# Kernel optimization log

Hardware: AMD Instinct MI355X
Metric: run time of the kernel (lower is better)

## Reference

```python
import jax, jax.numpy as jnp
import numpy as np

N = 100000       # nodes
DEG = 16         # in-degree per node
E = N * DEG      # edges
IN_DIM = 128
H_DIM = 128
NEG_SLOPE = 0.01  # F.leaky_relu default


def setup_inputs() -> dict:
    key = jax.random.key(0)
    ks = jax.random.split(key, 12)
    sc = 0.05
    attr = jax.random.normal(ks[0], (N, IN_DIM), jnp.float32)
    edge_d = jax.random.uniform(ks[1], (E, 1), dtype=jnp.float32)
    edge_src = jax.random.randint(ks[2], (E,), 0, N, dtype=jnp.int32)
    edge_dst = jnp.repeat(jnp.arange(N, dtype=jnp.int32), DEG)  # every node gets DEG msgs
    return {
        "attr": attr,
        "edge_d": edge_d,
        "W_V1": jax.random.normal(ks[3], (1, 1), jnp.float32) * sc,
        "W_W1": jax.random.normal(ks[4], (H_DIM, IN_DIM), jnp.float32) * sc,
        "W_U1": jax.random.normal(ks[5], (H_DIM, IN_DIM), jnp.float32) * sc,
        "W_a1": jax.random.normal(ks[6], (1, 2 * H_DIM + 1), jnp.float32) * sc,
        "W_V2": jax.random.normal(ks[7], (1, 1), jnp.float32) * sc,
        "W_W2": jax.random.normal(ks[8], (H_DIM, H_DIM), jnp.float32) * sc,
        "W_U2": jax.random.normal(ks[9], (H_DIM, H_DIM), jnp.float32) * sc,
        "W_a2": jax.random.normal(ks[10], (1, 2 * H_DIM + 1), jnp.float32) * sc,
        "edge_src": edge_src,
        "edge_dst": edge_dst,
    }


def gat_layer(h, edge_d, edge_src, edge_dst, W_V, W_W, W_U, W_a):
    n = h.shape[0]
    t = edge_d @ W_V.T                      # [E,1] edge feature transform (fcV)
    z = h @ W_W.T                           # [N,H] (fcW)
    z_i = h @ W_U.T                         # [N,H] (fcU)
    Hd = z.shape[1]
    a = W_a[0]                              # [2H+1]
    a_src, a_dst, a_t = a[:Hd], a[Hd:2 * Hd], a[2 * Hd:]
    # attn_fc(concat(z_src, z_dst, t)) decomposed into per-node scores + edge term
    s_src = z @ a_src                       # [N]
    s_dst = z @ a_dst                       # [N]
    e = s_src[edge_src] + s_dst[edge_dst] + (t @ a_t)  # [E]
    e = jax.nn.leaky_relu(e, NEG_SLOPE)
    # per-destination-node softmax over incoming edges (mailbox softmax)
    m = jax.ops.segment_max(e, edge_dst, num_segments=n)
    ex = jnp.exp(e - m[edge_dst])
    denom = jax.ops.segment_sum(ex, edge_dst, num_segments=n)
    alpha = ex / denom[edge_dst]            # [E]
    # weighted neighbor aggregation
    zn = jax.ops.segment_sum(alpha[:, None] * z[edge_src], edge_dst, num_segments=n)
    return jax.nn.relu(z_i + zn)


def reference(attr, edge_d, W_V1, W_W1, W_U1, W_a1, W_V2, W_W2, W_U2, W_a2,
              edge_src, edge_dst):
    h = gat_layer(attr, edge_d, edge_src, edge_dst, W_V1, W_W1, W_U1, W_a1)
    h = gat_layer(h, edge_d, edge_src, edge_dst, W_V2, W_W2, W_U2, W_a2)
    return h
```

## Files before the change

kernel.cpp:

```cpp
#include <hip/hip_runtime.h>

#define N_NODES 100000
#define DEG 16
#define DIM 128
#define NTILES 1563
#define T8 196
#define DGRID (T8 * 4 * 8)
#define LSTR 136

typedef short bf16x8 __attribute__((ext_vector_type(8)));
typedef float f32x4 __attribute__((ext_vector_type(4)));

__device__ __forceinline__ unsigned short f2bf(float f) {
    unsigned int u = __builtin_bit_cast(unsigned int, f);
    u = (u + 0x7fffu + ((u >> 16) & 1u)) >> 16;
    return (unsigned short)u;
}
__device__ __forceinline__ float bf2f(unsigned short h) {
    unsigned int u = ((unsigned int)h) << 16;
    return __builtin_bit_cast(float, u);
}
__device__ __forceinline__ bf16x8 pack_bf16x8(float4 lo, float4 hi) {
    bf16x8 f;
    f[0] = (short)f2bf(lo.x); f[1] = (short)f2bf(lo.y);
    f[2] = (short)f2bf(lo.z); f[3] = (short)f2bf(lo.w);
    f[4] = (short)f2bf(hi.x); f[5] = (short)f2bf(hi.y);
    f[6] = (short)f2bf(hi.z); f[7] = (short)f2bf(hi.w);
    return f;
}

__global__ __launch_bounds__(256) void prep_w(
    const float* __restrict__ W_W1, const float* __restrict__ W_U1,
    const float* __restrict__ W_W2, const float* __restrict__ W_U2,
    unsigned short* __restrict__ Wc1, unsigned short* __restrict__ Wc2)
{
    int idx = blockIdx.x * 256 + threadIdx.x;
    int half = idx & 32767;
    const float* src = (idx < 32768)
        ? (half < 16384 ? W_W1 + half : W_U1 + half - 16384)
        : (half < 16384 ? W_W2 + half : W_U2 + half - 16384);
    unsigned short* dst = (idx < 32768) ? Wc1 + half : Wc2 + half;
    *dst = f2bf(*src);
}

__global__ __launch_bounds__(256) void dense_tile(
    const float* __restrict__ hsrc,
    const unsigned short* __restrict__ Wc,
    const float* __restrict__ W_a,
    unsigned short* __restrict__ z,
    unsigned short* __restrict__ zi,
    float* __restrict__ s_src0, float* __restrict__ s_src1,
    float* __restrict__ s_dst0, float* __restrict__ s_dst1)
{
    __shared__ unsigned short Wt[64 * LSTR];
    __shared__ unsigned short Ht[64 * LSTR];

    const int bid = blockIdx.x;
    const int xcd = bid & 7;
    const int q = bid >> 3;
    const int cb = q & 3;
    const int tile = (q >> 2) * 8 + xcd;
    if (tile >= NTILES) return;
    const int nodebase = tile * 64;
    const int t = threadIdx.x;

    {
        int r = t >> 2, c0 = (t & 3) * 32;
        const unsigned short* src = Wc + (size_t)(cb * 64 + r) * DIM + c0;
        unsigned short* dst = Wt + r * LSTR + c0;
#pragma unroll
        for (int i = 0; i < 4; i++)
            *(uint4*)(dst + i * 8) = *(const uint4*)(src + i * 8);
    }
    {
        int r = t >> 2, c0 = (t & 3) * 32;
        int node = nodebase + r;
        unsigned short* dst = Ht + r * LSTR + c0;
        float4 v[8];
#pragma unroll
        for (int i = 0; i < 8; i++) v[i] = make_float4(0.f, 0.f, 0.f, 0.f);
        if (node < N_NODES) {
            const float* src = hsrc + (size_t)node * DIM + c0;
#pragma unroll
            for (int i = 0; i < 8; i++) v[i] = *(const float4*)(src + i * 4);
        }
#pragma unroll
        for (int i = 0; i < 4; i++)
            *(bf16x8*)(dst + i * 8) = pack_bf16x8(v[2 * i], v[2 * i + 1]);
    }
    __syncthreads();

    const int wave = t >> 6;
    const int lane = t & 63;
    const int n16 = lane & 15;
    const int quad = lane >> 4;
    const int node = nodebase + wave * 16 + n16;

    bf16x8 hfrag[4];
    const unsigned short* hrow = Ht + (wave * 16 + n16) * LSTR + quad * 8;
#pragma unroll
    for (int ks = 0; ks < 4; ks++)
        hfrag[ks] = *(const bf16x8*)(hrow + ks * 32);

    f32x4 acc[4];
#pragma unroll
    for (int ct = 0; ct < 4; ct++) {
        const unsigned short* wrow = Wt + (ct * 16 + n16) * LSTR + quad * 8;
        f32x4 a = {0.f, 0.f, 0.f, 0.f};
#pragma unroll
        for (int ks = 0; ks < 4; ks++)
            a = __builtin_amdgcn_mfma_f32_16x16x32_bf16(
                    *(const bf16x8*)(wrow + ks * 32), hfrag[ks], a, 0, 0, 0);
        acc[ct] = a;
    }

    if (node < N_NODES) {
        unsigned short* zout = (cb < 2 ? z : zi);
        unsigned short* orow = zout + (size_t)node * DIM + (cb & 1) * 64 + quad * 4;
#pragma unroll
        for (int ct = 0; ct < 4; ct++) {
            uint2 pk;
            pk.x = (unsigned int)f2bf(acc[ct][0]) | ((unsigned int)f2bf(acc[ct][1]) << 16);
            pk.y = (unsigned int)f2bf(acc[ct][2]) | ((unsigned int)f2bf(acc[ct][3]) << 16);
            *(uint2*)(orow + ct * 16) = pk;
        }
    }

    if (cb < 2) {
        float ps = 0.f, pd = 0.f;
#pragma unroll
        for (int ct = 0; ct < 4; ct++) {
            float4 as = *(const float4*)(W_a + cb * 64 + ct * 16 + quad * 4);
            float4 ad = *(const float4*)(W_a + DIM + cb * 64 + ct * 16 + quad * 4);
            ps += acc[ct][0] * as.x + acc[ct][1] * as.y
                + acc[ct][2] * as.z + acc[ct][3] * as.w;
            pd += acc[ct][0] * ad.x + acc[ct][1] * ad.y
                + acc[ct][2] * ad.z + acc[ct][3] * ad.w;
        }
        ps += __shfl_xor(ps, 16); ps += __shfl_xor(ps, 32);
        pd += __shfl_xor(pd, 16); pd += __shfl_xor(pd, 32);
        if (lane < 16 && node < N_NODES) {
            (cb == 0 ? s_src0 : s_src1)[node] = ps;
            (cb == 0 ? s_dst0 : s_dst1)[node] = pd;
        }
    }
}

__global__ __launch_bounds__(256) void aggr_dense(
    const unsigned short* __restrict__ z,
    const unsigned short* __restrict__ zi,
    const float* __restrict__ s_src0, const float* __restrict__ s_src1,
    const float* __restrict__ s_dst0, const float* __restrict__ s_dst1,
    const float* __restrict__ edge_d,
    const int* __restrict__ edge_src,
    const float* __restrict__ W_V,
    const float* __restrict__ W_a,
    const unsigned short* __restrict__ Wc2,
    const float* __restrict__ W_a2,
    unsigned short* __restrict__ z2,
    unsigned short* __restrict__ zi2,
    float* __restrict__ t_src0, float* __restrict__ t_src1,
    float* __restrict__ t_dst0, float* __restrict__ t_dst1)
{
    __shared__ unsigned short Hl[16 * LSTR];

    const int t = threadIdx.x;
    const int base = blockIdx.x * 16;
    const int nl = t >> 4;
    const int j  = t & 15;
    const int nodej = base + nl;
    const int lane = t & 63;
    const int gb = lane & 48;

    const int e = nodej * DEG + j;

    int   s  = __builtin_nontemporal_load(edge_src + e);
    float ed = __builtin_nontemporal_load(edge_d + e);

    float v_ss0 = s_src0[s];
    float v_ss1 = s_src1[s];
    float v_sd0 = s_dst0[nodej];
    float v_sd1 = s_dst1[nodej];

    const int c8 = j * 8;
    uint4 raw[DEG];
#pragma unroll
    for (int jj = 0; jj < DEG; jj++) {
        int sj = __shfl(s, gb | jj);
        raw[jj] = *(const uint4*)(z + (size_t)sj * DIM + c8);
    }
    uint4 zr = *(const uint4*)(zi + (size_t)nodej * DIM + c8);

    float coef = W_V[0] * W_a[2 * DIM];
    float x = (v_ss0 + v_ss1) + (v_sd0 + v_sd1) + ed * coef;
    x = x > 0.f ? x : 0.01f * x;
    float m = x;
    m = fmaxf(m, __shfl_xor(m, 1));
    m = fmaxf(m, __shfl_xor(m, 2));
    m = fmaxf(m, __shfl_xor(m, 4));
    m = fmaxf(m, __shfl_xor(m, 8));
    float ex = __expf(x - m);
    float d = ex;
    d += __shfl_xor(d, 1); d += __shfl_xor(d, 2);
    d += __shfl_xor(d, 4); d += __shfl_xor(d, 8);
    float aj = ex / d;

    float acc8[8] = {};
#pragma unroll
    for (int jj = 0; jj < DEG; jj++) {
        float a = __shfl(aj, gb | jj);
        acc8[0] += a * bf2f((unsigned short)raw[jj].x);
        acc8[1] += a * bf2f((unsigned short)(raw[jj].x >> 16));
        acc8[2] += a * bf2f((unsigned short)raw[jj].y);
        acc8[3] += a * bf2f((unsigned short)(raw[jj].y >> 16));
        acc8[4] += a * bf2f((unsigned short)raw[jj].z);
        acc8[5] += a * bf2f((unsigned short)(raw[jj].z >> 16));
        acc8[6] += a * bf2f((unsigned short)raw[jj].w);
        acc8[7] += a * bf2f((unsigned short)(raw[jj].w >> 16));
    }

    float v[8];
    v[0] = fmaxf(bf2f((unsigned short)zr.x) + acc8[0], 0.f);
    v[1] = fmaxf(bf2f((unsigned short)(zr.x >> 16)) + acc8[1], 0.f);
    v[2] = fmaxf(bf2f((unsigned short)zr.y) + acc8[2], 0.f);
    v[3] = fmaxf(bf2f((unsigned short)(zr.y >> 16)) + acc8[3], 0.f);
    v[4] = fmaxf(bf2f((unsigned short)zr.z) + acc8[4], 0.f);
    v[5] = fmaxf(bf2f((unsigned short)(zr.z >> 16)) + acc8[5], 0.f);
    v[6] = fmaxf(bf2f((unsigned short)zr.w) + acc8[6], 0.f);
    v[7] = fmaxf(bf2f((unsigned short)(zr.w >> 16)) + acc8[7], 0.f);

    {
        uint4 pk;
        pk.x = (unsigned int)f2bf(v[0]) | ((unsigned int)f2bf(v[1]) << 16);
        pk.y = (unsigned int)f2bf(v[2]) | ((unsigned int)f2bf(v[3]) << 16);
        pk.z = (unsigned int)f2bf(v[4]) | ((unsigned int)f2bf(v[5]) << 16);
        pk.w = (unsigned int)f2bf(v[6]) | ((unsigned int)f2bf(v[7]) << 16);
        *(uint4*)(Hl + nl * LSTR + c8) = pk;
    }
    __syncthreads();

    const int wave = t >> 6;
    const int n16 = lane & 15;
    const int quad = lane >> 4;
    const int node = base + n16;

    bf16x8 hfrag[4];
    const unsigned short* hrow = Hl + n16 * LSTR + quad * 8;
#pragma unroll
    for (int ks = 0; ks < 4; ks++)
        hfrag[ks] = *(const bf16x8*)(hrow + ks * 32);

    f32x4 acc[4];
#pragma unroll
    for (int ct = 0; ct < 4; ct++) {
        const unsigned short* wrow = Wc2 + (size_t)(wave * 64 + ct * 16 + n16) * DIM + quad * 8;
        f32x4 a = {0.f, 0.f, 0.f, 0.f};
#pragma unroll
        for (int ks = 0; ks < 4; ks++)
            a = __builtin_amdgcn_mfma_f32_16x16x32_bf16(
                    *(const bf16x8*)(wrow + ks * 32), hfrag[ks], a, 0, 0, 0);
        acc[ct] = a;
    }

    {
        unsigned short* zout = (wave < 2 ? z2 : zi2);
        unsigned short* orow = zout + (size_t)node * DIM + (wave & 1) * 64 + quad * 4;
#pragma unroll
        for (int ct = 0; ct < 4; ct++) {
            uint2 pk;
            pk.x = (unsigned int)f2bf(acc[ct][0]) | ((unsigned int)f2bf(acc[ct][1]) << 16);
            pk.y = (unsigned int)f2bf(acc[ct][2]) | ((unsigned int)f2bf(acc[ct][3]) << 16);
            *(uint2*)(orow + ct * 16) = pk;
        }
    }

    if (wave < 2) {
        float ps = 0.f, pd = 0.f;
#pragma unroll
        for (int ct = 0; ct < 4; ct++) {
            float4 as = *(const float4*)(W_a2 + wave * 64 + ct * 16 + quad * 4);
            float4 ad = *(const float4*)(W_a2 + DIM + wave * 64 + ct * 16 + quad * 4);
            ps += acc[ct][0] * as.x + acc[ct][1] * as.y
                + acc[ct][2] * as.z + acc[ct][3] * as.w;
            pd += acc[ct][0] * ad.x + acc[ct][1] * ad.y
                + acc[ct][2] * ad.z + acc[ct][3] * ad.w;
        }
        ps += __shfl_xor(ps, 16); ps += __shfl_xor(ps, 32);
        pd += __shfl_xor(pd, 16); pd += __shfl_xor(pd, 32);
        if (lane < 16) {
            (wave == 0 ? t_src0 : t_src1)[node] = ps;
            (wave == 0 ? t_dst0 : t_dst1)[node] = pd;
        }
    }
}

__global__ __launch_bounds__(256) void aggr_final(
    const unsigned short* __restrict__ z,
    const unsigned short* __restrict__ zi,
    const float* __restrict__ s_src0, const float* __restrict__ s_src1,
    const float* __restrict__ s_dst0, const float* __restrict__ s_dst1,
    const float* __restrict__ edge_d,
    const int* __restrict__ edge_src,
    const float* __restrict__ W_V,
    const float* __restrict__ W_a,
    float* __restrict__ out_f32)
{
    const int t = threadIdx.x;
    const int base = blockIdx.x * 16;
    const int nl = t >> 4;
    const int j  = t & 15;
    const int node = base + nl;
    const int lane = t & 63;
    const int gb = lane & 48;

    const int e = node * DEG + j;

    int   s  = __builtin_nontemporal_load(edge_src + e);
    float ed = __builtin_nontemporal_load(edge_d + e);

    float v_ss0 = s_src0[s];
    float v_ss1 = s_src1[s];
    float v_sd0 = s_dst0[node];
    float v_sd1 = s_dst1[node];

    const int c8 = j * 8;
    uint4 raw[DEG];
#pragma unroll
    for (int jj = 0; jj < DEG; jj++) {
        int sj = __shfl(s, gb | jj);
        raw[jj] = *(const uint4*)(z + (size_t)sj * DIM + c8);
    }
    uint4 zr = *(const uint4*)(zi + (size_t)node * DIM + c8);

    float coef = W_V[0] * W_a[2 * DIM];
    float x = (v_ss0 + v_ss1) + (v_sd0 + v_sd1) + ed * coef;
    x = x > 0.f ? x : 0.01f * x;
    float m = x;
    m = fmaxf(m, __shfl_xor(m, 1));
    m = fmaxf(m, __shfl_xor(m, 2));
    m = fmaxf(m, __shfl_xor(m, 4));
    m = fmaxf(m, __shfl_xor(m, 8));
    float ex = __expf(x - m);
    float d = ex;
    d += __shfl_xor(d, 1); d += __shfl_xor(d, 2);
    d += __shfl_xor(d, 4); d += __shfl_xor(d, 8);
    float aj = ex / d;

    float acc[8] = {};
#pragma unroll
    for (int jj = 0; jj < DEG; jj++) {
        float a = __shfl(aj, gb | jj);
        acc[0] += a * bf2f((unsigned short)raw[jj].x);
        acc[1] += a * bf2f((unsigned short)(raw[jj].x >> 16));
        acc[2] += a * bf2f((unsigned short)raw[jj].y);
        acc[3] += a * bf2f((unsigned short)(raw[jj].y >> 16));
        acc[4] += a * bf2f((unsigned short)raw[jj].z);
        acc[5] += a * bf2f((unsigned short)(raw[jj].z >> 16));
        acc[6] += a * bf2f((unsigned short)raw[jj].w);
        acc[7] += a * bf2f((unsigned short)(raw[jj].w >> 16));
    }

    float* op = out_f32 + (size_t)node * DIM + c8;
    f32x4 o0, o1;
    o0[0] = fmaxf(bf2f((unsigned short)zr.x) + acc[0], 0.f);
    o0[1] = fmaxf(bf2f((unsigned short)(zr.x >> 16)) + acc[1], 0.f);
    o0[2] = fmaxf(bf2f((unsigned short)zr.y) + acc[2], 0.f);
    o0[3] = fmaxf(bf2f((unsigned short)(zr.y >> 16)) + acc[3], 0.f);
    o1[0] = fmaxf(bf2f((unsigned short)zr.z) + acc[4], 0.f);
    o1[1] = fmaxf(bf2f((unsigned short)(zr.z >> 16)) + acc[5], 0.f);
    o1[2] = fmaxf(bf2f((unsigned short)zr.w) + acc[6], 0.f);
    o1[3] = fmaxf(bf2f((unsigned short)(zr.w >> 16)) + acc[7], 0.f);
    __builtin_nontemporal_store(o0, (f32x4*)op);
    __builtin_nontemporal_store(o1, (f32x4*)(op + 4));
}

extern "C" void kernel_launch(void* const* d_in, const int* in_sizes, int n_in,
                              void* d_out, int out_size, void* d_ws, size_t ws_size,
                              hipStream_t stream) {
    const float* attr     = (const float*)d_in[0];
    const float* edge_d   = (const float*)d_in[1];
    const float* W_V1     = (const float*)d_in[2];
    const float* W_W1     = (const float*)d_in[3];
    const float* W_U1     = (const float*)d_in[4];
    const float* W_a1     = (const float*)d_in[5];
    const float* W_V2     = (const float*)d_in[6];
    const float* W_W2     = (const float*)d_in[7];
    const float* W_U2     = (const float*)d_in[8];
    const float* W_a2     = (const float*)d_in[9];
    const int*   edge_src = (const int*)d_in[10];

    float* out = (float*)d_out;

    char* ws = (char*)d_ws;
    unsigned short* z1  = (unsigned short*)ws;
    unsigned short* zi1 = (unsigned short*)(ws + 26u * 1024 * 1024);
    unsigned short* z2  = (unsigned short*)(ws + 52u * 1024 * 1024);
    unsigned short* zi2 = (unsigned short*)(ws + 78u * 1024 * 1024);
    unsigned short* Wc1 = (unsigned short*)(ws + 104u * 1024 * 1024);
    unsigned short* Wc2 = (unsigned short*)(ws + 105u * 1024 * 1024);
    float* s_src0       = (float*)(ws + 106u * 1024 * 1024);
    float* s_src1       = (float*)(ws + 107u * 1024 * 1024);
    float* s_dst0       = (float*)(ws + 108u * 1024 * 1024);
    float* s_dst1       = (float*)(ws + 109u * 1024 * 1024);
    float* t_src0       = (float*)(ws + 110u * 1024 * 1024);
    float* t_src1       = (float*)(ws + 111u * 1024 * 1024);
    float* t_dst0       = (float*)(ws + 112u * 1024 * 1024);
    float* t_dst1       = (float*)(ws + 113u * 1024 * 1024);

    prep_w<<<256, 256, 0, stream>>>(W_W1, W_U1, W_W2, W_U2, Wc1, Wc2);

    dense_tile<<<DGRID, 256, 0, stream>>>(attr, Wc1, W_a1, z1, zi1,
                                          s_src0, s_src1, s_dst0, s_dst1);

    aggr_dense<<<6250, 256, 0, stream>>>(z1, zi1, s_src0, s_src1, s_dst0, s_dst1,
                                         edge_d, edge_src, W_V1, W_a1,
                                         Wc2, W_a2, z2, zi2,
                                         t_src0, t_src1, t_dst0, t_dst1);

    aggr_final<<<6250, 256, 0, stream>>>(z2, zi2, t_src0, t_src1, t_dst0, t_dst1,
                                         edge_d, edge_src, W_V2, W_a2, out);
}
```

Before: 321.7 us.

## Pre-convert attr to bf16 in prep kernel and load MFMA fragments directly from global

A combined prep kernel now converts the whole fp32 attr matrix to a padded bf16 buffer alongside the weight conversion, which is itself vectorised to 8 elements per thread. The dense kernel then reads bf16 H fragments straight from global memory instead of staging converted fp32 rows through shared memory. Because each node tile is handled by four column-block blocks, attr was previously read and converted four times in fp32; the intent is to cut that redundant traffic and shared-memory staging. The cost is an extra full pass that writes attr as bf16, plus reusing that buffer as z2.

Result: no change. 321.9 us (+0.1%).

```diff
diff --git a/kernel.cpp b/kernel.cpp
--- a/kernel.cpp
+++ b/kernel.cpp
@@ -1,11 +1,12 @@
 #include <hip/hip_runtime.h>
 
 #define N_NODES 100000
+#define NPAD 100032
 #define DEG 16
 #define DIM 128
+#define E_EDGES 1600000
 #define NTILES 1563
-#define T8 196
-#define DGRID (T8 * 4 * 8)
+#define DGRID (196 * 4 * 8)
 #define LSTR 136
 
 typedef short bf16x8 __attribute__((ext_vector_type(8)));
@@ -29,22 +30,43 @@
     return f;
 }
 
-__global__ __launch_bounds__(256) void prep_w(
+__global__ __launch_bounds__(256) void prep_all(
+    const float* __restrict__ attr,
     const float* __restrict__ W_W1, const float* __restrict__ W_U1,
     const float* __restrict__ W_W2, const float* __restrict__ W_U2,
+    unsigned short* __restrict__ attrb,
     unsigned short* __restrict__ Wc1, unsigned short* __restrict__ Wc2)
 {
-    int idx = blockIdx.x * 256 + threadIdx.x;
-    int half = idx & 32767;
-    const float* src = (idx < 32768)
-        ? (half < 16384 ? W_W1 + half : W_U1 + half - 16384)
-        : (half < 16384 ? W_W2 + half : W_U2 + half - 16384);
-    unsigned short* dst = (idx < 32768) ? Wc1 + half : Wc2 + half;
-    *dst = f2bf(*src);
-}
-
-__global__ __launch_bounds__(256) void dense_tile(
-    const float* __restrict__ hsrc,
+    const int b = blockIdx.x;
+    const int t = threadIdx.x;
+    if (b < 6252) {
+        size_t g = (size_t)b * 2048 + (size_t)t * 8;
+        float4 v0 = make_float4(0.f, 0.f, 0.f, 0.f);
+        float4 v1 = v0;
+        if (g < (size_t)N_NODES * DIM) {
+            v0 = *(const float4*)(attr + g);
+            v1 = *(const float4*)(attr + g + 4);
+        }
+        *(bf16x8*)(attrb + g) = pack_bf16x8(v0, v1);
+    } else if (b < 6284) {
+        int g = (b - 6252) * 2048 + t * 8;
+        int half = g & 32767;
+        const float* src = (g < 32768)
+            ? (half < 16384 ? W_W1 + half : W_U1 + (half - 16384))
+            : (half < 16384 ? W_W2 + half : W_U2 + (half - 16384));
+        unsigned short* dst = (g < 32768) ? Wc1 + half : Wc2 + half;
+        float4 v0 = *(const float4*)(src);
+        float4 v1 = *(const float4*)(src + 4);
+        *(bf16x8*)(dst) = pack_bf16x8(v0, v1);
+    } else {
+        unsigned short* p = attrb + (size_t)N_NODES * DIM;
+        *(uint4*)(p + t * 16) = make_uint4(0, 0, 0, 0);
+        *(uint4*)(p + t * 16 + 8) = make_uint4(0, 0, 0, 0);
+    }
+}
+
+__global__ __launch_bounds__(256) void dense_g(
+    const unsigned short* __restrict__ hsrc,
     const unsigned short* __restrict__ Wc,
     const float* __restrict__ W_a,
     unsigned short* __restrict__ z,
@@ -53,7 +75,6 @@
     float* __restrict__ s_dst0, float* __restrict__ s_dst1)
 {
     __shared__ unsigned short Wt[64 * LSTR];
-    __shared__ unsigned short Ht[64 * LSTR];
 
     const int bid = blockIdx.x;
     const int xcd = bid & 7;
@@ -63,33 +84,6 @@
     if (tile >= NTILES) return;
     const int nodebase = tile * 64;
     const int t = threadIdx.x;
-
-    {
-        int r = t >> 2, c0 = (t & 3) * 32;
-        const unsigned short* src = Wc + (size_t)(cb * 64 + r) * DIM + c0;
-        unsigned short* dst = Wt + r * LSTR + c0;
-#pragma unroll
-        for (int i = 0; i < 4; i++)
-            *(uint4*)(dst + i * 8) = *(const uint4*)(src + i * 8);
-    }
-    {
-        int r = t >> 2, c0 = (t & 3) * 32;
-        int node = nodebase + r;
-        unsigned short* dst = Ht + r * LSTR + c0;
-        float4 v[8];
-#pragma unroll
-        for (int i = 0; i < 8; i++) v[i] = make_float4(0.f, 0.f, 0.f, 0.f);
-        if (node < N_NODES) {
-            const float* src = hsrc + (size_t)node * DIM + c0;
-#pragma unroll
-            for (int i = 0; i < 8; i++) v[i] = *(const float4*)(src + i * 4);
-        }
-#pragma unroll
-        for (int i = 0; i < 4; i++)
-            *(bf16x8*)(dst + i * 8) = pack_bf16x8(v[2 * i], v[2 * i + 1]);
-    }
-    __syncthreads();
-
     const int wave = t >> 6;
     const int lane = t & 63;
     const int n16 = lane & 15;
@@ -97,10 +91,20 @@
     const int node = nodebase + wave * 16 + n16;
 
     bf16x8 hfrag[4];
-    const unsigned short* hrow = Ht + (wave * 16 + n16) * LSTR + quad * 8;
+    const unsigned short* hrow = hsrc + (size_t)node * DIM + quad * 8;
 #pragma unroll
     for (int ks = 0; ks < 4; ks++)
         hfrag[ks] = *(const bf16x8*)(hrow + ks * 32);
+
+    {
+        int r = t >> 2, c0 = (t & 3) * 32;
+        const unsigned short* src = Wc + (size_t)(cb * 64 + r) * DIM + c0;
+        unsigned short* dst = Wt + r * LSTR + c0;
+#pragma unroll
+        for (int i = 0; i < 4; i++)
+            *(uint4*)(dst + i * 8) = *(const uint4*)(src + i * 8);
+    }
+    __syncthreads();
 
     f32x4 acc[4];
 #pragma unroll
@@ -392,25 +396,27 @@
     float* out = (float*)d_out;
 
     char* ws = (char*)d_ws;
-    unsigned short* z1  = (unsigned short*)ws;
-    unsigned short* zi1 = (unsigned short*)(ws + 26u * 1024 * 1024);
-    unsigned short* z2  = (unsigned short*)(ws + 52u * 1024 * 1024);
-    unsigned short* zi2 = (unsigned short*)(ws + 78u * 1024 * 1024);
-    unsigned short* Wc1 = (unsigned short*)(ws + 104u * 1024 * 1024);
-    unsigned short* Wc2 = (unsigned short*)(ws + 105u * 1024 * 1024);
-    float* s_src0       = (float*)(ws + 106u * 1024 * 1024);
-    float* s_src1       = (float*)(ws + 107u * 1024 * 1024);
-    float* s_dst0       = (float*)(ws + 108u * 1024 * 1024);
-    float* s_dst1       = (float*)(ws + 109u * 1024 * 1024);
-    float* t_src0       = (float*)(ws + 110u * 1024 * 1024);
-    float* t_src1       = (float*)(ws + 111u * 1024 * 1024);
-    float* t_dst0       = (float*)(ws + 112u * 1024 * 1024);
-    float* t_dst1       = (float*)(ws + 113u * 1024 * 1024);
-
-    prep_w<<<256, 256, 0, stream>>>(W_W1, W_U1, W_W2, W_U2, Wc1, Wc2);
-
-    dense_tile<<<DGRID, 256, 0, stream>>>(attr, Wc1, W_a1, z1, zi1,
-                                          s_src0, s_src1, s_dst0, s_dst1);
+    unsigned short* attrb = (unsigned short*)ws;
+    unsigned short* z1    = (unsigned short*)(ws + 26u * 1024 * 1024);
+    unsigned short* zi1   = (unsigned short*)(ws + 52u * 1024 * 1024);
+    unsigned short* zi2   = (unsigned short*)(ws + 78u * 1024 * 1024);
+    unsigned short* Wc1   = (unsigned short*)(ws + 104u * 1024 * 1024);
+    unsigned short* Wc2   = (unsigned short*)(ws + 105u * 1024 * 1024);
+    float* s_src0         = (float*)(ws + 106u * 1024 * 1024);
+    float* s_src1         = (float*)(ws + 107u * 1024 * 1024);
+    float* s_dst0         = (float*)(ws + 108u * 1024 * 1024);
+    float* s_dst1         = (float*)(ws + 109u * 1024 * 1024);
+    float* t_src0         = (float*)(ws + 110u * 1024 * 1024);
+    float* t_src1         = (float*)(ws + 111u * 1024 * 1024);
+    float* t_dst0         = (float*)(ws + 112u * 1024 * 1024);
+    float* t_dst1         = (float*)(ws + 113u * 1024 * 1024);
+    unsigned short* z2    = attrb;
+
+    prep_all<<<6285, 256, 0, stream>>>(attr, W_W1, W_U1, W_W2, W_U2,
+                                       attrb, Wc1, Wc2);
+
+    dense_g<<<DGRID, 256, 0, stream>>>(attrb, Wc1, W_a1, z1, zi1,
+                                       s_src0, s_src1, s_dst0, s_dst1);
 
     aggr_dense<<<6250, 256, 0, stream>>>(z1, zi1, s_src0, s_src1, s_dst0, s_dst1,
                                          edge_d, edge_src, W_V1, W_a1,
```
